# Kernel optimization log

Measured on AMD Instinct MI355X. Metric: run time of the kernel, lower is better.

## Reference

```python
import jax, jax.numpy as jnp
import numpy as np

B, S, HID = 1, 2048, 1024
NH, NKV, HD = 16, 4, 64
SCALING = 0.125  # attention_multiplier = 1/sqrt(head_dim)
ROPE_THETA = 10000.0
NEG_MIN = jnp.finfo(jnp.float32).min


def rotate_half(x):
    x1, x2 = jnp.split(x, 2, axis=-1)
    return jnp.concatenate([-x2, x1], axis=-1)


def setup_inputs() -> dict:
    key = jax.random.key(0)
    ks = jax.random.split(key, 6)
    hidden_states = jax.random.normal(ks[0], (B, S, HID), dtype=jnp.float32)
    # RoPE tables: [1, 1, S, HD]
    inv_freq = 1.0 / (ROPE_THETA ** (np.arange(0, HD, 2, dtype=np.float32) / HD))
    t = np.arange(S, dtype=np.float32)
    freqs = np.outer(t, inv_freq)                      # [S, HD/2]
    emb = np.concatenate([freqs, freqs], axis=-1)      # [S, HD]
    cos = jnp.asarray(np.cos(emb))[None, None]
    sin = jnp.asarray(np.sin(emb))[None, None]
    attention_mask = jnp.ones((B, S), dtype=bool)
    sc = 0.02
    Wq = jax.random.normal(ks[1], (HID, NH * HD), dtype=jnp.float32) * sc
    Wk = jax.random.normal(ks[2], (HID, NKV * HD), dtype=jnp.float32) * sc
    Wv = jax.random.normal(ks[3], (HID, NKV * HD), dtype=jnp.float32) * sc
    Wo = jax.random.normal(ks[4], (NH * HD, HID), dtype=jnp.float32) * sc
    return {"hidden_states": hidden_states, "cos": cos, "sin": sin,
            "attention_mask": attention_mask, "Wq": Wq, "Wk": Wk, "Wv": Wv, "Wo": Wo}


def reference(hidden_states, cos, sin, attention_mask, Wq, Wk, Wv, Wo):
    b, s, _ = hidden_states.shape
    # projections -> [B, H, S, D]
    q = (hidden_states @ Wq).reshape(b, s, NH, HD).transpose(0, 2, 1, 3)
    k = (hidden_states @ Wk).reshape(b, s, NKV, HD).transpose(0, 2, 1, 3)
    v = (hidden_states @ Wv).reshape(b, s, NKV, HD).transpose(0, 2, 1, 3)
    # RoPE (full head_dim rotation; cos/sin broadcast over batch/heads)
    q = q * cos + rotate_half(q) * sin
    k = k * cos + rotate_half(k) * sin
    # repeat_kv: expand kv heads to match query heads
    n_rep = NH // NKV
    k = jnp.repeat(k, n_rep, axis=1)
    v = jnp.repeat(v, n_rep, axis=1)
    # scores: [B, H, Sq, Sk]
    attn = jnp.einsum('bhqd,bhkd->bhqk', q, k) * SCALING
    mask = attention_mask[:, None, None, :].astype(attn.dtype)  # bool padding mask
    attn = attn + (1.0 - mask) * NEG_MIN
    attn = jax.nn.softmax(attn.astype(jnp.float32), axis=-1).astype(q.dtype)
    out = jnp.einsum('bhqk,bhkd->bhqd', attn, v)
    out = out.transpose(0, 2, 1, 3).reshape(b, s, NH * HD)
    return out @ Wo
```

## Files before the change

kernel.cpp:

```cpp
#include <hip/hip_runtime.h>
#include <stdint.h>

typedef __attribute__((ext_vector_type(8))) short short8;
typedef __attribute__((ext_vector_type(4))) short short4v;
typedef __attribute__((ext_vector_type(4))) float floatx4;
typedef __attribute__((ext_vector_type(2))) unsigned int uint2v;

#define AS1 __attribute__((address_space(1)))
#define AS3 __attribute__((address_space(3)))

__device__ __forceinline__ void async16(const void* g, void* l) {
  __builtin_amdgcn_global_load_lds((const AS1 unsigned int*)g, (AS3 unsigned int*)l, 16, 0, 0);
}

__device__ __forceinline__ short f2bf(float f) {
  unsigned u = __float_as_uint(f);
  u = (u + 0x7FFF + ((u >> 16) & 1)) >> 16;
  return (short)u;
}

__device__ __forceinline__ unsigned f2bf2(float lo, float hi) {
  return __builtin_amdgcn_perm(__float_as_uint(hi) + 0x8000u,
                               __float_as_uint(lo) + 0x8000u, 0x07060302u);
}

__device__ __forceinline__ void stage_sw(const short* src, int stride,
                                         short* tile, int cb, int lane) {
  int i = cb + lane;
  int r = i >> 3, j = i & 7;
  async16(src + (size_t)r * stride + ((j ^ (r & 7)) * 8), tile + cb * 8);
}
__device__ __forceinline__ int sw(int row, int c8) {
  return row * 64 + ((c8 ^ (row & 7)) * 8);
}

__global__ void k_prep(const float* __restrict__ X, const float* __restrict__ Wq,
                       const float* __restrict__ Wk, const float* __restrict__ Wv,
                       const float* __restrict__ Wo, short* __restrict__ Xb,
                       short* __restrict__ Wqkvt, short* __restrict__ Wot) {
  int b = blockIdx.x, tid = threadIdx.x;
  if (b < 2048) {
    int i = b * 1024 + tid * 4;
    floatx4 v = *(const floatx4*)(X + i);
    short4v o;
    o.x = f2bf(v.x); o.y = f2bf(v.y); o.z = f2bf(v.z); o.w = f2bf(v.w);
    *(short4v*)(Xb + i) = o;
    return;
  }
  const float* src; short* dst; int N, brel, rowoff;
  if (b < 3072)      { src = Wq; dst = Wqkvt; N = 1024; brel = b - 2048; rowoff = 0; }
  else if (b < 3328) { src = Wk; dst = Wqkvt; N = 256;  brel = b - 3072; rowoff = 1024; }
  else if (b < 3584) { src = Wv; dst = Wqkvt; N = 256;  brel = b - 3328; rowoff = 1280; }
  else               { src = Wo; dst = Wot;   N = 1024; brel = b - 3584; rowoff = 0; }
  __shared__ short t[32][33];
  int nt = N >> 5;
  int n0 = (brel % nt) * 32, k0 = (brel / nt) * 32;
  int tx = tid & 31, ty = tid >> 5;
#pragma unroll
  for (int i = 0; i < 4; i++)
    t[ty + 8 * i][tx] = f2bf(src[(size_t)(k0 + ty + 8 * i) * N + n0 + tx]);
  __syncthreads();
#pragma unroll
  for (int i = 0; i < 4; i++)
    dst[(size_t)(rowoff + n0 + ty + 8 * i) * 1024 + k0 + tx] = t[tx][ty + 8 * i];
}

__global__ __launch_bounds__(256) void k_gemmqkv(const short* __restrict__ A,
                                                 const short* __restrict__ Bt,
                                                 short* __restrict__ Qb,
                                                 short* __restrict__ Kb,
                                                 short* __restrict__ Vtb,
                                                 const float* __restrict__ cosp,
                                                 const float* __restrict__ sinp,
                                                 float qscale) {
  int tid = threadIdx.x;
  int w = tid >> 6, lane = tid & 63, quad = lane >> 4, l16 = lane & 15;
  __shared__ short As[64 * 64];
  __shared__ short Bs[128 * 64];
  const int K = 1024;
  const short* Ag = A + (size_t)(blockIdx.y * 64) * K;
  const short* Bg = Bt + (size_t)(blockIdx.x * 128) * K;
  int hw = w & 1;
  int dlo = (w >> 1) * 16 + l16;
  floatx4 acc[4][2] = {};
  for (int kk = 0; kk < K; kk += 64) {
    __syncthreads();
#pragma unroll
    for (int t = 0; t < 2; t++) stage_sw(Ag + kk, K, As, (w * 2 + t) * 64, lane);
#pragma unroll
    for (int t = 0; t < 4; t++) stage_sw(Bg + kk, K, Bs, (w * 4 + t) * 64, lane);
    __syncthreads();
#pragma unroll
    for (int ks = 0; ks < 2; ks++) {
      short8 af[4], bfr[2];
#pragma unroll
      for (int i = 0; i < 4; i++)
        af[i] = *(const short8*)&As[sw(i * 16 + l16, ks * 4 + quad)];
#pragma unroll
      for (int j = 0; j < 2; j++)
        bfr[j] = *(const short8*)&Bs[sw(hw * 64 + j * 32 + (w >> 1) * 16 + l16, ks * 4 + quad)];
#pragma unroll
      for (int i = 0; i < 4; i++)
#pragma unroll
        for (int j = 0; j < 2; j++)
          acc[i][j] = __builtin_amdgcn_mfma_f32_16x16x32_bf16(af[i], bfr[j], acc[i][j], 0, 0, 0);
    }
  }
  int bx = blockIdx.x, by = blockIdx.y;
  if (bx < 10) {
    short* dst; float scale;
    if (bx < 8) { dst = Qb + (size_t)(bx * 2 + hw) * 2048 * 64; scale = qscale; }
    else        { dst = Kb + (size_t)((bx - 8) * 2 + hw) * 2048 * 64; scale = 1.0f; }
#pragma unroll
    for (int i = 0; i < 4; i++)
#pragma unroll
      for (int r = 0; r < 4; r++) {
        int s = by * 64 + i * 16 + quad * 4 + r;
        float c = cosp[s * 64 + dlo], sn = sinp[s * 64 + dlo];
        float v0 = acc[i][0][r], v1 = acc[i][1][r];
        dst[(size_t)s * 64 + dlo]      = f2bf((v0 * c - v1 * sn) * scale);
        dst[(size_t)s * 64 + 32 + dlo] = f2bf((v1 * c + v0 * sn) * scale);
      }
  } else {
    short* dst = Vtb + (size_t)((bx - 10) * 2 + hw) * 64 * 2048;
#pragma unroll
    for (int j = 0; j < 2; j++) {
      int d = j * 32 + dlo;
#pragma unroll
      for (int i = 0; i < 4; i++) {
        short4v pk;
#pragma unroll
        for (int r = 0; r < 4; r++) pk[r] = f2bf(acc[i][j][r]);
        *(short4v*)&dst[(size_t)d * 2048 + by * 64 + i * 16 + quad * 4] = pk;
      }
    }
  }
}

__global__ __launch_bounds__(256) void k_gemm(const short* __restrict__ A,
                                              const short* __restrict__ Bt,
                                              float* __restrict__ C,
                                              int M, int N, int K) {
  int tid = threadIdx.x;
  int w = tid >> 6, lane = tid & 63, quad = lane >> 4, l16 = lane & 15;
  __shared__ short As[64 * 64];
  __shared__ short Bs[128 * 64];
  const short* Ag = A + (size_t)(blockIdx.y * 64) * K;
  const short* Bg = Bt + (size_t)(blockIdx.x * 128) * K;
  floatx4 acc[4][2] = {};
  for (int kk = 0; kk < K; kk += 64) {
    __syncthreads();
#pragma unroll
    for (int t = 0; t < 2; t++) stage_sw(Ag + kk, K, As, (w * 2 + t) * 64, lane);
#pragma unroll
    for (int t = 0; t < 4; t++) stage_sw(Bg + kk, K, Bs, (w * 4 + t) * 64, lane);
    __syncthreads();
#pragma unroll
    for (int ks = 0; ks < 2; ks++) {
      short8 af[4], bfr[2];
#pragma unroll
      for (int i = 0; i < 4; i++)
        af[i] = *(const short8*)&As[sw(i * 16 + l16, ks * 4 + quad)];
#pragma unroll
      for (int j = 0; j < 2; j++)
        bfr[j] = *(const short8*)&Bs[sw(w * 32 + j * 16 + l16, ks * 4 + quad)];
#pragma unroll
      for (int i = 0; i < 4; i++)
#pragma unroll
        for (int j = 0; j < 2; j++)
          acc[i][j] = __builtin_amdgcn_mfma_f32_16x16x32_bf16(af[i], bfr[j], acc[i][j], 0, 0, 0);
    }
  }
#pragma unroll
  for (int i = 0; i < 4; i++)
#pragma unroll
    for (int j = 0; j < 2; j++)
#pragma unroll
      for (int r = 0; r < 4; r++) {
        int row = blockIdx.y * 64 + i * 16 + quad * 4 + r;
        int col = blockIdx.x * 128 + w * 32 + j * 16 + l16;
        C[(size_t)row * N + col] = acc[i][j][r];
      }
}

__global__ __launch_bounds__(256) void k_attn(const short* __restrict__ Qb,
                                              const short* __restrict__ Kb,
                                              const short* __restrict__ Vt,
                                              float* __restrict__ Opart,
                                              float* __restrict__ lpart) {
  int qt = blockIdx.x;
  int h = blockIdx.y;
  int sp = blockIdx.z;
  int kvh = h >> 2;
  int tid = threadIdx.x, w = tid >> 6, lane = tid & 63, quad = lane >> 4, l16 = lane & 15;
  __shared__ short Ks[2][4096];
  __shared__ short Vs[2][4096];
  __shared__ short Ps[4][32 * 72];
  const short* Qg = Qb + ((size_t)h * 2048 + qt * 128 + w * 32) * 64;
  const short* Kg0 = Kb + ((size_t)kvh * 2048 + sp * 1024) * 64;
  const short* Vg0 = Vt + (size_t)kvh * 64 * 2048 + sp * 1024;
  short8 qf[2][2];
#pragma unroll
  for (int q2 = 0; q2 < 2; q2++)
#pragma unroll
    for (int ks = 0; ks < 2; ks++)
      qf[q2][ks] = *(const short8*)(Qg + (q2 * 16 + l16) * 64 + ks * 32 + quad * 8);
#pragma unroll
  for (int t = 0; t < 2; t++) stage_sw(Kg0, 64, Ks[0], (w * 2 + t) * 64, lane);
#pragma unroll
  for (int t = 0; t < 2; t++) stage_sw(Vg0, 2048, Vs[0], (w * 2 + t) * 64, lane);
  floatx4 accO[2][4] = {};
  float lsum[2] = {0.f, 0.f};
  short* myPs = Ps[w];
  for (int kt = 0; kt < 16; kt++) {
    __syncthreads();
    if (kt + 1 < 16) {
      int nb = (kt + 1) & 1;
#pragma unroll
      for (int t = 0; t < 2; t++)
        stage_sw(Kg0 + (kt + 1) * 4096, 64, Ks[nb], (w * 2 + t) * 64, lane);
#pragma unroll
      for (int t = 0; t < 2; t++)
        stage_sw(Vg0 + (kt + 1) * 64, 2048, Vs[nb], (w * 2 + t) * 64, lane);
    }
    int cbuf = kt & 1;
    floatx4 accS[2][4] = {};
#pragma unroll
    for (int ks = 0; ks < 2; ks++)
#pragma unroll
      for (int mt = 0; mt < 4; mt++) {
        short8 af = *(const short8*)&Ks[cbuf][sw(mt * 16 + l16, ks * 4 + quad)];
#pragma unroll
        for (int q2 = 0; q2 < 2; q2++)
          accS[q2][mt] = __builtin_amdgcn_mfma_f32_16x16x32_bf16(af, qf[q2][ks], accS[q2][mt], 0, 0, 0);
      }
#pragma unroll
    for (int q2 = 0; q2 < 2; q2++)
#pragma unroll
      for (int mt = 0; mt < 4; mt++) {
        float p0 = __builtin_amdgcn_exp2f(accS[q2][mt][0]);
        float p1 = __builtin_amdgcn_exp2f(accS[q2][mt][1]);
        float p2 = __builtin_amdgcn_exp2f(accS[q2][mt][2]);
        float p3 = __builtin_amdgcn_exp2f(accS[q2][mt][3]);
        lsum[q2] += (p0 + p1) + (p2 + p3);
        uint2v pk;
        pk.x = f2bf2(p0, p1);
        pk.y = f2bf2(p2, p3);
        *(uint2v*)&myPs[(q2 * 16 + l16) * 72 + mt * 16 + quad * 4] = pk;
      }
    asm volatile("s_waitcnt lgkmcnt(0)" ::: "memory");
#pragma unroll
    for (int ks = 0; ks < 2; ks++) {
      short8 pf[2];
#pragma unroll
      for (int q2 = 0; q2 < 2; q2++)
        pf[q2] = *(const short8*)&myPs[(q2 * 16 + l16) * 72 + ks * 32 + quad * 8];
#pragma unroll
      for (int dt = 0; dt < 4; dt++) {
        short8 vf = *(const short8*)&Vs[cbuf][sw(dt * 16 + l16, ks * 4 + quad)];
#pragma unroll
        for (int q2 = 0; q2 < 2; q2++)
          accO[q2][dt] = __builtin_amdgcn_mfma_f32_16x16x32_bf16(pf[q2], vf, accO[q2][dt], 0, 0, 0);
      }
    }
  }
  float* Op = Opart + (size_t)sp * 2048 * 1024;
#pragma unroll
  for (int q2 = 0; q2 < 2; q2++) {
    float ls = lsum[q2];
    ls += __shfl_xor(ls, 16);
    ls += __shfl_xor(ls, 32);
    if (lane < 16)
      lpart[(size_t)sp * 16 * 2048 + h * 2048 + qt * 128 + w * 32 + q2 * 16 + lane] = ls;
#pragma unroll
    for (int dt = 0; dt < 4; dt++)
#pragma unroll
      for (int r = 0; r < 4; r++) {
        int srow = qt * 128 + w * 32 + q2 * 16 + quad * 4 + r;
        int col = h * 64 + dt * 16 + l16;
        Op[(size_t)srow * 1024 + col] = accO[q2][dt][r];
      }
  }
}

__global__ void k_comb(const float* __restrict__ Opart, const float* __restrict__ lpart,
                       short* __restrict__ AOb) {
  int idx = (blockIdx.x * 256 + threadIdx.x) * 4;
  int s = idx >> 10, h = (idx & 1023) >> 6;
  float l = lpart[h * 2048 + s] + lpart[16 * 2048 + h * 2048 + s];
  float inv = 1.0f / l;
  floatx4 a = *(const floatx4*)(Opart + idx);
  floatx4 b = *(const floatx4*)(Opart + 2048 * 1024 + idx);
  uint2v pk;
  pk.x = f2bf2((a.x + b.x) * inv, (a.y + b.y) * inv);
  pk.y = f2bf2((a.z + b.z) * inv, (a.w + b.w) * inv);
  *(uint2v*)&AOb[idx] = pk;
}

extern "C" void kernel_launch(void* const* d_in, const int* in_sizes, int n_in,
                              void* d_out, int out_size, void* d_ws, size_t ws_size,
                              hipStream_t stream) {
  const float* X    = (const float*)d_in[0];
  const float* cosp = (const float*)d_in[1];
  const float* sinp = (const float*)d_in[2];
  const float* Wq = (const float*)d_in[4];
  const float* Wk = (const float*)d_in[5];
  const float* Wv = (const float*)d_in[6];
  const float* Wo = (const float*)d_in[7];
  float* out = (float*)d_out;

  short* Xb    = (short*)d_ws;
  short* Wqkvt = Xb + 2097152;
  short* Wot   = Wqkvt + 1572864;
  short* Qb2   = Wot + 1048576;
  short* Kb2   = Qb2 + 2097152;
  short* Vtb   = Kb2 + 524288;
  short* AOb   = Vtb + 524288;
  float* Opart = (float*)(AOb + 2097152);
  float* lpart = Opart + 2 * 2097152;

  const float QSCALE = 0.125f * 1.44269504088896340736f;

  k_prep<<<4608, 256, 0, stream>>>(X, Wq, Wk, Wv, Wo, Xb, Wqkvt, Wot);
  k_gemmqkv<<<dim3(12, 32), 256, 0, stream>>>(Xb, Wqkvt, Qb2, Kb2, Vtb, cosp, sinp, QSCALE);
  k_attn<<<dim3(16, 16, 2), 256, 0, stream>>>(Qb2, Kb2, Vtb, Opart, lpart);
  k_comb<<<2048, 256, 0, stream>>>(Opart, lpart, AOb);
  k_gemm<<<dim3(8, 32), 256, 0, stream>>>(AOb, Wot, out, 2048, 1024, 1024);
}
```

Before: 149.1 us.

## Double-buffer GEMM LDS staging and split attention KV range four ways

Both projection GEMMs now double-buffer their LDS tiles, prefetching the next K slice while computing the current one, and need one barrier per iteration instead of two. The attention kernel splits the key/value sequence into four chunks instead of two, which doubles the grid to raise occupancy across CUs. The combine kernel is extended to sum four partial outputs and normalizers. This doubles LDS use in the GEMMs and doubles the partial-output traffic through the combine step. The no-max softmax relies on bounded scores, as before.

```diff
diff --git a/kernel.cpp b/kernel.cpp
--- a/kernel.cpp
+++ b/kernel.cpp
@@ -75,30 +75,36 @@
                                                  float qscale) {
   int tid = threadIdx.x;
   int w = tid >> 6, lane = tid & 63, quad = lane >> 4, l16 = lane & 15;
-  __shared__ short As[64 * 64];
-  __shared__ short Bs[128 * 64];
+  __shared__ short As[2][4096];
+  __shared__ short Bs[2][8192];
   const int K = 1024;
   const short* Ag = A + (size_t)(blockIdx.y * 64) * K;
   const short* Bg = Bt + (size_t)(blockIdx.x * 128) * K;
   int hw = w & 1;
   int dlo = (w >> 1) * 16 + l16;
   floatx4 acc[4][2] = {};
-  for (int kk = 0; kk < K; kk += 64) {
+#pragma unroll
+  for (int t = 0; t < 2; t++) stage_sw(Ag, K, As[0], (w * 2 + t) * 64, lane);
+#pragma unroll
+  for (int t = 0; t < 4; t++) stage_sw(Bg, K, Bs[0], (w * 4 + t) * 64, lane);
+  for (int kt = 0; kt < 16; kt++) {
     __syncthreads();
-#pragma unroll
-    for (int t = 0; t < 2; t++) stage_sw(Ag + kk, K, As, (w * 2 + t) * 64, lane);
-#pragma unroll
-    for (int t = 0; t < 4; t++) stage_sw(Bg + kk, K, Bs, (w * 4 + t) * 64, lane);
-    __syncthreads();
+    int cur = kt & 1, nxt = cur ^ 1;
+    if (kt + 1 < 16) {
+#pragma unroll
+      for (int t = 0; t < 2; t++) stage_sw(Ag + (kt + 1) * 64, K, As[nxt], (w * 2 + t) * 64, lane);
+#pragma unroll
+      for (int t = 0; t < 4; t++) stage_sw(Bg + (kt + 1) * 64, K, Bs[nxt], (w * 4 + t) * 64, lane);
+    }
 #pragma unroll
     for (int ks = 0; ks < 2; ks++) {
       short8 af[4], bfr[2];
 #pragma unroll
       for (int i = 0; i < 4; i++)
-        af[i] = *(const short8*)&As[sw(i * 16 + l16, ks * 4 + quad)];
+        af[i] = *(const short8*)&As[cur][sw(i * 16 + l16, ks * 4 + quad)];
 #pragma unroll
       for (int j = 0; j < 2; j++)
-        bfr[j] = *(const short8*)&Bs[sw(hw * 64 + j * 32 + (w >> 1) * 16 + l16, ks * 4 + quad)];
+        bfr[j] = *(const short8*)&Bs[cur][sw(hw * 64 + j * 32 + (w >> 1) * 16 + l16, ks * 4 + quad)];
 #pragma unroll
       for (int i = 0; i < 4; i++)
 #pragma unroll
@@ -143,27 +149,34 @@
                                               int M, int N, int K) {
   int tid = threadIdx.x;
   int w = tid >> 6, lane = tid & 63, quad = lane >> 4, l16 = lane & 15;
-  __shared__ short As[64 * 64];
-  __shared__ short Bs[128 * 64];
+  __shared__ short As[2][4096];
+  __shared__ short Bs[2][8192];
   const short* Ag = A + (size_t)(blockIdx.y * 64) * K;
   const short* Bg = Bt + (size_t)(blockIdx.x * 128) * K;
   floatx4 acc[4][2] = {};
-  for (int kk = 0; kk < K; kk += 64) {
+  int kiters = K >> 6;
+#pragma unroll
+  for (int t = 0; t < 2; t++) stage_sw(Ag, K, As[0], (w * 2 + t) * 64, lane);
+#pragma unroll
+  for (int t = 0; t < 4; t++) stage_sw(Bg, K, Bs[0], (w * 4 + t) * 64, lane);
+  for (int kt = 0; kt < kiters; kt++) {
     __syncthreads();
-#pragma unroll
-    for (int t = 0; t < 2; t++) stage_sw(Ag + kk, K, As, (w * 2 + t) * 64, lane);
-#pragma unroll
-    for (int t = 0; t < 4; t++) stage_sw(Bg + kk, K, Bs, (w * 4 + t) * 64, lane);
-    __syncthreads();
+    int cur = kt & 1, nxt = cur ^ 1;
+    if (kt + 1 < kiters) {
+#pragma unroll
+      for (int t = 0; t < 2; t++) stage_sw(Ag + (kt + 1) * 64, K, As[nxt], (w * 2 + t) * 64, lane);
+#pragma unroll
+      for (int t = 0; t < 4; t++) stage_sw(Bg + (kt + 1) * 64, K, Bs[nxt], (w * 4 + t) * 64, lane);
+    }
 #pragma unroll
     for (int ks = 0; ks < 2; ks++) {
       short8 af[4], bfr[2];
 #pragma unroll
       for (int i = 0; i < 4; i++)
-        af[i] = *(const short8*)&As[sw(i * 16 + l16, ks * 4 + quad)];
+        af[i] = *(const short8*)&As[cur][sw(i * 16 + l16, ks * 4 + quad)];
 #pragma unroll
       for (int j = 0; j < 2; j++)
-        bfr[j] = *(const short8*)&Bs[sw(w * 32 + j * 16 + l16, ks * 4 + quad)];
+        bfr[j] = *(const short8*)&Bs[cur][sw(w * 32 + j * 16 + l16, ks * 4 + quad)];
 #pragma unroll
       for (int i = 0; i < 4; i++)
 #pragma unroll
@@ -197,8 +210,8 @@
   __shared__ short Vs[2][4096];
   __shared__ short Ps[4][32 * 72];
   const short* Qg = Qb + ((size_t)h * 2048 + qt * 128 + w * 32) * 64;
-  const short* Kg0 = Kb + ((size_t)kvh * 2048 + sp * 1024) * 64;
-  const short* Vg0 = Vt + (size_t)kvh * 64 * 2048 + sp * 1024;
+  const short* Kg0 = Kb + ((size_t)kvh * 2048 + sp * 512) * 64;
+  const short* Vg0 = Vt + (size_t)kvh * 64 * 2048 + sp * 512;
   short8 qf[2][2];
 #pragma unroll
   for (int q2 = 0; q2 < 2; q2++)
@@ -212,9 +225,9 @@
   floatx4 accO[2][4] = {};
   float lsum[2] = {0.f, 0.f};
   short* myPs = Ps[w];
-  for (int kt = 0; kt < 16; kt++) {
+  for (int kt = 0; kt < 8; kt++) {
     __syncthreads();
-    if (kt + 1 < 16) {
+    if (kt + 1 < 8) {
       int nb = (kt + 1) & 1;
 #pragma unroll
       for (int t = 0; t < 2; t++)
@@ -287,13 +300,19 @@
                        short* __restrict__ AOb) {
   int idx = (blockIdx.x * 256 + threadIdx.x) * 4;
   int s = idx >> 10, h = (idx & 1023) >> 6;
-  float l = lpart[h * 2048 + s] + lpart[16 * 2048 + h * 2048 + s];
+  float l = 0.f;
+#pragma unroll
+  for (int sp = 0; sp < 4; sp++) l += lpart[sp * 16 * 2048 + h * 2048 + s];
   float inv = 1.0f / l;
   floatx4 a = *(const floatx4*)(Opart + idx);
-  floatx4 b = *(const floatx4*)(Opart + 2048 * 1024 + idx);
+#pragma unroll
+  for (int sp = 1; sp < 4; sp++) {
+    floatx4 b = *(const floatx4*)(Opart + (size_t)sp * 2048 * 1024 + idx);
+    a.x += b.x; a.y += b.y; a.z += b.z; a.w += b.w;
+  }
   uint2v pk;
-  pk.x = f2bf2((a.x + b.x) * inv, (a.y + b.y) * inv);
-  pk.y = f2bf2((a.z + b.z) * inv, (a.w + b.w) * inv);
+  pk.x = f2bf2(a.x * inv, a.y * inv);
+  pk.y = f2bf2(a.z * inv, a.w * inv);
   *(uint2v*)&AOb[idx] = pk;
 }
 
@@ -317,13 +336,13 @@
   short* Vtb   = Kb2 + 524288;
   short* AOb   = Vtb + 524288;
   float* Opart = (float*)(AOb + 2097152);
-  float* lpart = Opart + 2 * 2097152;
+  float* lpart = Opart + 4 * 2097152;
 
   const float QSCALE = 0.125f * 1.44269504088896340736f;
 
   k_prep<<<4608, 256, 0, stream>>>(X, Wq, Wk, Wv, Wo, Xb, Wqkvt, Wot);
   k_gemmqkv<<<dim3(12, 32), 256, 0, stream>>>(Xb, Wqkvt, Qb2, Kb2, Vtb, cosp, sinp, QSCALE);
-  k_attn<<<dim3(16, 16, 2), 256, 0, stream>>>(Qb2, Kb2, Vtb, Opart, lpart);
+  k_attn<<<dim3(16, 16, 4), 256, 0, stream>>>(Qb2, Kb2, Vtb, Opart, lpart);
   k_comb<<<2048, 256, 0, stream>>>(Opart, lpart, AOb);
   k_gemm<<<dim3(8, 32), 256, 0, stream>>>(AOb, Wot, out, 2048, 1024, 1024);
 }
```

Result: slower. 153.5 us (+2.9%).
